# Performance work log

Measured on AMD Instinct MI355X. Metric: run time of the kernel, lower is better.

Reference implementation:

```python
import jax, jax.numpy as jnp
import numpy as np

N_ENT = 100000   # n_entities
N_HE = 20000     # n_hyperedges
D = 128          # embed_dim (in_dim == out_dim)
NNZ_A = 1600000  # nnz of A_in (~16 per row)
NNZ_H = 1000000  # nnz of each hyperedge incidence matrix


def spmm(rows, cols, vals, x, n_rows):
    """COO sparse (n_rows, n_cols) @ dense x (n_cols, D) -> (n_rows, D)."""
    msgs = vals[:, None] * x[cols]  # [nnz, D] gather + scale
    return jax.ops.segment_sum(msgs, rows, num_segments=n_rows)


def setup_inputs() -> dict:
    key = jax.random.key(0)
    ks = jax.random.split(key, 18)
    ego = jax.random.normal(ks[0], (N_ENT, D), dtype=jnp.float32)
    a_rows = jax.random.randint(ks[1], (NNZ_A,), 0, N_ENT)
    a_cols = jax.random.randint(ks[2], (NNZ_A,), 0, N_ENT)
    a_vals = jax.random.uniform(ks[3], (NNZ_A,), dtype=jnp.float32)
    p1_rows = jax.random.randint(ks[4], (NNZ_H,), 0, N_HE)
    p1_cols = jax.random.randint(ks[5], (NNZ_H,), 0, N_ENT)
    p1_vals = jax.random.uniform(ks[6], (NNZ_H,), dtype=jnp.float32)
    p2_rows = jax.random.randint(ks[7], (NNZ_H,), 0, N_ENT)
    p2_cols = jax.random.randint(ks[8], (NNZ_H,), 0, N_HE)
    p2_vals = jax.random.uniform(ks[9], (NNZ_H,), dtype=jnp.float32)
    l1_rows = jax.random.randint(ks[10], (NNZ_H,), 0, N_HE)
    l1_cols = jax.random.randint(ks[11], (NNZ_H,), 0, N_ENT)
    l1_vals = jax.random.uniform(ks[12], (NNZ_H,), dtype=jnp.float32)
    l2_rows = jax.random.randint(ks[13], (NNZ_H,), 0, N_ENT)
    l2_cols = jax.random.randint(ks[14], (NNZ_H,), 0, N_HE)
    l2_vals = jax.random.uniform(ks[15], (NNZ_H,), dtype=jnp.float32)
    W1 = jax.random.normal(ks[16], (D, D), dtype=jnp.float32) * 0.05
    b1 = jnp.zeros((D,), dtype=jnp.float32)
    W2 = jax.random.normal(ks[17], (D, D), dtype=jnp.float32) * 0.05
    b2 = jnp.zeros((D,), dtype=jnp.float32)
    return dict(ego=ego, a_rows=a_rows, a_cols=a_cols, a_vals=a_vals,
                p1_rows=p1_rows, p1_cols=p1_cols, p1_vals=p1_vals,
                p2_rows=p2_rows, p2_cols=p2_cols, p2_vals=p2_vals,
                l1_rows=l1_rows, l1_cols=l1_cols, l1_vals=l1_vals,
                l2_rows=l2_rows, l2_cols=l2_cols, l2_vals=l2_vals,
                W1=W1, b1=b1, W2=W2, b2=b2)


def reference(ego, a_rows, a_cols, a_vals,
              p1_rows, p1_cols, p1_vals,
              p2_rows, p2_cols, p2_vals,
              l1_rows, l1_cols, l1_vals,
              l2_rows, l2_cols, l2_vals,
              W1, b1, W2, b2):
    # side = A_in @ ego
    side = spmm(a_rows, a_cols, a_vals, ego, N_ENT)
    # proj = norm_proj2 @ (norm_proj1 @ ego)
    proj = spmm(p2_rows, p2_cols, p2_vals,
                spmm(p1_rows, p1_cols, p1_vals, ego, N_HE), N_ENT)
    # lib = norm_lib2 @ (norm_lib1 @ ego)
    lib = spmm(l2_rows, l2_cols, l2_vals,
               spmm(l1_rows, l1_cols, l1_vals, ego, N_HE), N_ENT)
    side = side + proj + lib
    # bi-interaction aggregator (PyTorch Linear: x @ W.T + b), LeakyReLU slope 0.01
    sum_emb = jax.nn.leaky_relu((ego + side) @ W1.T + b1)
    bi_emb = jax.nn.leaky_relu((ego * side) @ W2.T + b2)
    # attention=True -> sum of both branches; dropout is identity in eval
    return sum_emb + bi_emb
```

## Files before the change

### kernel.cpp

```cpp
#include <hip/hip_runtime.h>

#define N_ENT 100000
#define N_HE  20000
#define DD    128

#define RB_A   0
#define RB_P1  100000
#define RB_P2  120000
#define RB_L1  220000
#define RB_L2  240000
#define NROWS_TOT 340000

#define NB 452
#define TILE 3072
#define EPT  12

typedef float f32x4 __attribute__((ext_vector_type(4)));
typedef short bf16x8 __attribute__((ext_vector_type(8)));

__device__ __forceinline__ int bucket_region(int b) {
    return (b < 98) ? 0 : (b < 177) ? 1 : (b < 275) ? 2 : (b < 354) ? 3 : 4;
}
__device__ __forceinline__ int seg_shift(int s)      { return (s == 1 || s == 3) ? 8 : 10; }
__device__ __forceinline__ int seg_bucketbase(int s) { return s == 0 ? 0 : s == 1 ? 98 : s == 2 ? 177 : s == 3 ? 275 : 354; }
__device__ __forceinline__ int seg_cap(int s)        { return s == 0 ? 17408 : (s == 1 || s == 3) ? 13824 : 11264; }
__device__ __forceinline__ long long seg_arenabase(int s) {
    return s == 0 ? 0LL : s == 1 ? 1705984LL : s == 2 ? 2798080LL : s == 3 ? 3901952LL : 4994048LL;
}
__device__ __forceinline__ int seg_rowbase(int s)    { return s == 0 ? 0 : s == 1 ? 100000 : s == 2 ? 120000 : s == 3 ? 220000 : 240000; }
__device__ __forceinline__ int seg_rows(int s)       { return (s == 1 || s == 3) ? 20000 : 100000; }

__device__ __forceinline__ float bf_lo(unsigned u) { return __uint_as_float(u << 16); }
__device__ __forceinline__ float bf_hi(unsigned u) { return __uint_as_float(u & 0xffff0000u); }
__device__ __forceinline__ unsigned short f2bf(float f) {
    unsigned u = __float_as_uint(f);
    unsigned r = (u + 0x7fffu + ((u >> 16) & 1u)) >> 16;
    return (unsigned short)r;
}
__device__ __forceinline__ unsigned pack_bf16(float a, float b) {
    return (unsigned)f2bf(a) | ((unsigned)f2bf(b) << 16);
}
__device__ __forceinline__ float lrelu(float x) { return x > 0.0f ? x : 0.01f * x; }
__device__ __forceinline__ float i8f(unsigned u, int b) {
    return (float)((int)(u << (24 - 8 * b)) >> 24);
}

__global__ __launch_bounds__(256) void quant_ego_kernel(
    const float* __restrict__ ego, unsigned* __restrict__ ego_q,
    float* __restrict__ ego_scale)
{
    int row = (blockIdx.x * 256 + threadIdx.x) >> 5;
    if (row >= N_ENT) return;
    int l = threadIdx.x & 31;
    const float4 v = *(const float4*)(ego + (long long)row * DD + l * 4);
    float m = fmaxf(fmaxf(fabsf(v.x), fabsf(v.y)), fmaxf(fabsf(v.z), fabsf(v.w)));
    for (int d = 1; d < 32; d <<= 1) m = fmaxf(m, __shfl_xor(m, d, 32));
    float inv = (m > 0.0f) ? 127.0f / m : 0.0f;
    int q0 = __float2int_rn(v.x * inv);
    int q1 = __float2int_rn(v.y * inv);
    int q2 = __float2int_rn(v.z * inv);
    int q3 = __float2int_rn(v.w * inv);
    unsigned pk = (q0 & 255) | ((q1 & 255) << 8) | ((q2 & 255) << 16) | ((q3 & 255) << 24);
    ego_q[row * 32 + l] = pk;
    if (l == 0) ego_scale[row] = m * (1.0f / 127.0f);
}

struct BuildArgs {
    const int*   rows[5];
    const int*   cols[5];
    const float* vals[5];
    int nnzbase[6];
};

__device__ __forceinline__ void seg_of(int i, const int* nnzbase, int& seg, int& li) {
    int s = 0;
    s += (i >= nnzbase[1]);
    s += (i >= nnzbase[2]);
    s += (i >= nnzbase[3]);
    s += (i >= nnzbase[4]);
    seg = s; li = i - nnzbase[s];
}

__global__ __launch_bounds__(256, 4) void partition_kernel(
    BuildArgs a, int* __restrict__ gcursor, int2* __restrict__ arena)
{
    __shared__ int2 staging[TILE];
    __shared__ unsigned short posb[TILE];
    __shared__ int  hist[NB];
    __shared__ int  excl[NB + 1];
    __shared__ int  cursor[NB];
    __shared__ int  gofs[NB];

    const int t = threadIdx.x;
    const int tile_base = blockIdx.x * TILE;
    const int total = a.nnzbase[5];
    int tile_n = total - tile_base;
    if (tile_n > TILE) tile_n = TILE;
    if (tile_n <= 0) return;

    for (int i = t; i < NB; i += 256) hist[i] = 0;
    __syncthreads();

    int pk[EPT];
#pragma unroll
    for (int q = 0; q < EPT; ++q) {
        int j = t + q * 256;
        pk[q] = -1;
        if (j < tile_n) {
            int i = tile_base + j;
            int seg, li; seg_of(i, a.nnzbase, seg, li);
            int row = a.rows[seg][li];
            int sh = seg_shift(seg);
            int b = seg_bucketbase(seg) + (row >> sh);
            int rl = row & ((1 << sh) - 1);
            pk[q] = (b << 10) | rl;
            atomicAdd(&hist[b], 1);
        }
    }
    __syncthreads();

    if (t < 64) {
        int carry = 0;
        for (int base = 0; base < NB; base += 64) {
            int idx = base + t;
            int v = (idx < NB) ? hist[idx] : 0;
            int inc = v;
            for (int d = 1; d < 64; d <<= 1) {
                int u = __shfl_up(inc, d, 64);
                if (t >= d) inc += u;
            }
            if (idx < NB) excl[idx] = carry + inc - v;
            carry += __shfl(inc, 63, 64);
        }
        if (t == 0) excl[NB] = carry;
    }
    __syncthreads();

    for (int b = t; b < NB; b += 256) {
        int c = hist[b];
        int e = excl[b];
        int gb = (c > 0) ? atomicAdd(&gcursor[b], c) : 0;
        cursor[b] = e;
        gofs[b] = gb - e;
    }
    __syncthreads();

#pragma unroll
    for (int q = 0; q < EPT; ++q) {
        int j = t + q * 256;
        if (j < tile_n) {
            int i = tile_base + j;
            int seg, li; seg_of(i, a.nnzbase, seg, li);
            int col = a.cols[seg][li];
            float v = a.vals[seg][li];
            int b = pk[q] >> 10;
            int rl = pk[q] & 1023;
            int pos = atomicAdd(&cursor[b], 1);
            staging[pos] = make_int2((rl << 17) | col, __float_as_int(v));
        }
    }
    __syncthreads();

    for (int b = t; b < NB; b += 256) {
        int lo = excl[b], hi = excl[b + 1];
        for (int p = lo; p < hi; ++p) posb[p] = (unsigned short)b;
    }
    __syncthreads();

    for (int p = t; p < tile_n; p += 256) {
        int b = posb[p];
        int reg = bucket_region(b);
        long long slot = seg_arenabase(reg) + (long long)(b - seg_bucketbase(reg)) * seg_cap(reg);
        arena[slot + gofs[b] + p] = staging[p];
    }
}

__global__ __launch_bounds__(512) void bucket_scan_kernel(
    const int* __restrict__ gcursor, int* __restrict__ bbase, int* __restrict__ rp)
{
    __shared__ int tmp[512];
    int t = threadIdx.x;
    int v = (t < NB) ? gcursor[t] : 0;
    tmp[t] = v;
    __syncthreads();
    for (int d = 1; d < 512; d <<= 1) {
        int u = (t >= d) ? tmp[t - d] : 0;
        __syncthreads();
        tmp[t] += u;
        __syncthreads();
    }
    if (t < NB) bbase[t] = tmp[t] - v;
    if (t == NB - 1) rp[NROWS_TOT] = tmp[t];
}

__global__ __launch_bounds__(256) void bucket_sort_kernel(
    const int* __restrict__ gcursor, const int* __restrict__ bbase,
    const int2* __restrict__ arena, const float* __restrict__ ego_scale,
    int2* __restrict__ cv, int* __restrict__ rp)
{
    __shared__ int hist[1024];
    __shared__ int excl[1024];
    __shared__ int wsum[4];

    const int b = blockIdx.x;
    const int t = threadIdx.x;
    const int reg = bucket_region(b);
    const int sh = seg_shift(reg);
    const int stride = 1 << sh;
    const int lb = b - seg_bucketbase(reg);
    const int row_base_local = lb << sh;
    int nrows = seg_rows(reg) - row_base_local;
    if (nrows > stride) nrows = stride;
    const long long slot = seg_arenabase(reg) + (long long)lb * seg_cap(reg);
    const int count = gcursor[b];
    const int fbase = bbase[b];
    const bool fold = (reg == 0) || (reg == 1) || (reg == 3);

    for (int i = t; i < 1024; i += 256) hist[i] = 0;
    __syncthreads();

    for (int j = t; j < count; j += 256) {
        int key = arena[slot + j].x;
        atomicAdd(&hist[key >> 17], 1);
    }
    __syncthreads();

    {
        const int lane = t & 63, wave = t >> 6;
        int v[4]; int s = 0;
#pragma unroll
        for (int q = 0; q < 4; ++q) { v[q] = hist[t * 4 + q]; s += v[q]; }
        int inc = s;
        for (int d = 1; d < 64; d <<= 1) {
            int u = __shfl_up(inc, d, 64);
            if (lane >= d) inc += u;
        }
        if (lane == 63) wsum[wave] = inc;
        __syncthreads();
        int woff = 0;
        for (int w = 0; w < wave; ++w) woff += wsum[w];
        int run = woff + inc - s;
#pragma unroll
        for (int q = 0; q < 4; ++q) { excl[t * 4 + q] = run; run += v[q]; }
    }
    __syncthreads();

    const int grow0 = seg_rowbase(reg) + row_base_local;
    for (int r = t; r < nrows; r += 256)
        rp[grow0 + r] = fbase + excl[r];
    __syncthreads();

    for (int j = t; j < count; j += 256) {
        int2 e = arena[slot + j];
        int r = e.x >> 17;
        int c = e.x & 0x1FFFF;
        float v = __int_as_float(e.y);
        if (fold) v *= ego_scale[c];
        int pos = atomicAdd(&excl[r], 1);
        cv[fbase + pos] = make_int2(c, __float_as_int(v));
    }
}

__device__ __forceinline__ void walk_row_i8(
    const int2* __restrict__ cv, int start, int end, int lane,
    const unsigned* __restrict__ xq, float* acc)
{
    const int g  = lane >> 4;
    const int p8 = (lane & 15) * 2;

    for (int sb = start; sb < end; sb += 64) {
        int nn = end - sb; if (nn > 64) nn = 64;
        int2 mycv = make_int2(0, 0);
        if (lane < nn) mycv = cv[sb + lane];
        const int nn1 = nn - 1;
#pragma unroll 2
        for (int jb = 0; jb < nn; jb += 4) {
            int idx  = jb + g;
            int idxc = idx < nn1 ? idx : nn1;
            int   cs = __shfl(mycv.x, idxc, 64);
            float vs = __shfl(__int_as_float(mycv.y), idxc, 64);
            vs = (idx <= nn1) ? vs : 0.0f;
            const uint2 u = *reinterpret_cast<const uint2*>(xq + cs * 32 + p8);
            acc[0] = fmaf(vs, i8f(u.x, 0), acc[0]);
            acc[1] = fmaf(vs, i8f(u.x, 1), acc[1]);
            acc[2] = fmaf(vs, i8f(u.x, 2), acc[2]);
            acc[3] = fmaf(vs, i8f(u.x, 3), acc[3]);
            acc[4] = fmaf(vs, i8f(u.y, 0), acc[4]);
            acc[5] = fmaf(vs, i8f(u.y, 1), acc[5]);
            acc[6] = fmaf(vs, i8f(u.y, 2), acc[6]);
            acc[7] = fmaf(vs, i8f(u.y, 3), acc[7]);
        }
    }
}

__device__ __forceinline__ void walk_row_bf(
    const int2* __restrict__ cv, int start, int end, int lane,
    const unsigned* __restrict__ xb, float* acc)
{
    const int g   = lane >> 4;
    const int p16 = (lane & 15) * 4;

    for (int sb = start; sb < end; sb += 64) {
        int nn = end - sb; if (nn > 64) nn = 64;
        int2 mycv = make_int2(0, 0);
        if (lane < nn) mycv = cv[sb + lane];
        const int nn1 = nn - 1;
#pragma unroll 2
        for (int jb = 0; jb < nn; jb += 4) {
            int idx  = jb + g;
            int idxc = idx < nn1 ? idx : nn1;
            int   cs = __shfl(mycv.x, idxc, 64);
            float vs = __shfl(__int_as_float(mycv.y), idxc, 64);
            vs = (idx <= nn1) ? vs : 0.0f;
            const uint4 u = *reinterpret_cast<const uint4*>(xb + cs * 64 + p16);
            acc[0] = fmaf(vs, bf_lo(u.x), acc[0]);
            acc[1] = fmaf(vs, bf_hi(u.x), acc[1]);
            acc[2] = fmaf(vs, bf_lo(u.y), acc[2]);
            acc[3] = fmaf(vs, bf_hi(u.y), acc[3]);
            acc[4] = fmaf(vs, bf_lo(u.z), acc[4]);
            acc[5] = fmaf(vs, bf_hi(u.z), acc[5]);
            acc[6] = fmaf(vs, bf_lo(u.w), acc[6]);
            acc[7] = fmaf(vs, bf_hi(u.w), acc[7]);
        }
    }
}

__device__ __forceinline__ void reduce_groups(float* acc)
{
#pragma unroll
    for (int e = 0; e < 8; ++e) {
        acc[e] += __shfl_xor(acc[e], 16, 64);
        acc[e] += __shfl_xor(acc[e], 32, 64);
    }
}

__global__ __launch_bounds__(256) void spmm_stage1_kernel(
    const int* __restrict__ rp, const int2* __restrict__ cv,
    const unsigned* __restrict__ ego_q,
    unsigned* __restrict__ h1, unsigned* __restrict__ h2)
{
    int wid = (blockIdx.x * 256 + threadIdx.x) >> 6;
    int lane = threadIdx.x & 63;
    if (wid >= 2 * N_HE) return;
    int rbase; unsigned* y;
    if (wid < N_HE) { rbase = RB_P1 + wid;           y = h1 + wid * 64; }
    else            { rbase = RB_L1 + (wid - N_HE);  y = h2 + (wid - N_HE) * 64; }

    float acc[8] = {0, 0, 0, 0, 0, 0, 0, 0};
    walk_row_i8(cv, rp[rbase], rp[rbase + 1], lane, ego_q, acc);
    reduce_groups(acc);

    if (lane < 16) {
        uint4 o;
        o.x = pack_bf16(acc[0], acc[1]);
        o.y = pack_bf16(acc[2], acc[3]);
        o.z = pack_bf16(acc[4], acc[5]);
        o.w = pack_bf16(acc[6], acc[7]);
        *reinterpret_cast<uint4*>(y + lane * 4) = o;
    }
}

__global__ __launch_bounds__(256) void spmm_stage2_kernel(
    const int* __restrict__ rp, const int2* __restrict__ cv,
    const unsigned* __restrict__ ego_q,
    const unsigned* __restrict__ h1, const unsigned* __restrict__ h2,
    float* __restrict__ side)
{
    int wid = (blockIdx.x * 256 + threadIdx.x) >> 6;
    int lane = threadIdx.x & 63;
    if (wid >= N_ENT) return;

    float acc[8] = {0, 0, 0, 0, 0, 0, 0, 0};
    walk_row_i8(cv, rp[RB_A  + wid], rp[RB_A  + wid + 1], lane, ego_q, acc);
    walk_row_bf(cv, rp[RB_P2 + wid], rp[RB_P2 + wid + 1], lane, h1, acc);
    walk_row_bf(cv, rp[RB_L2 + wid], rp[RB_L2 + wid + 1], lane, h2, acc);
    reduce_groups(acc);

    if (lane < 16) {
        float* yp = side + (long long)wid * DD + (lane & 15) * 8;
        float4 a0 = make_float4(acc[0], acc[1], acc[2], acc[3]);
        float4 a1 = make_float4(acc[4], acc[5], acc[6], acc[7]);
        *reinterpret_cast<float4*>(yp)     = a0;
        *reinterpret_cast<float4*>(yp + 4) = a1;
    }
}

union BfFrag { unsigned u[4]; bf16x8 v; };

__global__ __launch_bounds__(512, 4) void dense_mfma_kernel(
    const float* __restrict__ ego, const float* __restrict__ side,
    const float* __restrict__ W1, const float* __restrict__ b1,
    const float* __restrict__ W2, const float* __restrict__ b2,
    float* __restrict__ out)
{
    __shared__ unsigned Wb1[8192];
    __shared__ unsigned Wb2[8192];

    const int tid = threadIdx.x;

    for (int idx = tid; idx < 8192; idx += 512) {
        int row = idx >> 6, pc = idx & 63;
        unsigned pk1 = pack_bf16(W1[row * 128 + pc * 2], W1[row * 128 + pc * 2 + 1]);
        unsigned pk2 = pack_bf16(W2[row * 128 + pc * 2], W2[row * 128 + pc * 2 + 1]);
        int boff = row * 256 + ((pc * 4) ^ ((row & 7) << 4));
        *(unsigned*)((char*)Wb1 + boff) = pk1;
        *(unsigned*)((char*)Wb2 + boff) = pk2;
    }
    __syncthreads();

    const int wave = tid >> 6;
    const int lane = tid & 63;
    const int m    = lane & 15;
    const int kg   = lane >> 4;

    float bs[8], bb[8];
#pragma unroll
    for (int c = 0; c < 8; ++c) {
        bs[c] = b1[c * 16 + m];
        bb[c] = b2[c * 16 + m];
    }

    for (int wt = blockIdx.x * 8 + wave; wt < 6250; wt += gridDim.x * 8) {
        const long long r0 = (long long)(wt * 16 + m) * DD;

        f32x4 accS[8], accB[8];
#pragma unroll
        for (int c = 0; c < 8; ++c) { accS[c] = (f32x4)0.0f; accB[c] = (f32x4)0.0f; }

#pragma unroll 1
        for (int kk = 0; kk < 4; ++kk) {
            const int kb = kk * 32 + kg * 8;

            float4 ea = *(const float4*)(ego  + r0 + kb);
            float4 eb = *(const float4*)(ego  + r0 + kb + 4);
            float4 sa = *(const float4*)(side + r0 + kb);
            float4 sb = *(const float4*)(side + r0 + kb + 4);

            BfFrag aS, aB;
            aS.u[0] = pack_bf16(ea.x + sa.x, ea.y + sa.y);
            aS.u[1] = pack_bf16(ea.z + sa.z, ea.w + sa.w);
            aS.u[2] = pack_bf16(eb.x + sb.x, eb.y + sb.y);
            aS.u[3] = pack_bf16(eb.z + sb.z, eb.w + sb.w);
            aB.u[0] = pack_bf16(ea.x * sa.x, ea.y * sa.y);
            aB.u[1] = pack_bf16(ea.z * sa.z, ea.w * sa.w);
            aB.u[2] = pack_bf16(eb.x * sb.x, eb.y * sb.y);
            aB.u[3] = pack_bf16(eb.z * sb.z, eb.w * sb.w);

#pragma unroll
            for (int c = 0; c < 8; ++c) {
                int wrow = c * 16 + m;
                int boff = wrow * 256 + ((kk * 64 + (kg << 4)) ^ ((wrow & 7) << 4));
                bf16x8 w1 = *(const bf16x8*)((const char*)Wb1 + boff);
                bf16x8 w2 = *(const bf16x8*)((const char*)Wb2 + boff);
                accS[c] = __builtin_amdgcn_mfma_f32_16x16x32_bf16(aS.v, w1, accS[c], 0, 0, 0);
                accB[c] = __builtin_amdgcn_mfma_f32_16x16x32_bf16(aB.v, w2, accB[c], 0, 0, 0);
            }
        }

#pragma unroll
        for (int c = 0; c < 8; ++c) {
#pragma unroll
            for (int q = 0; q < 4; ++q) {
                int orow = wt * 16 + kg * 4 + q;
                out[(long long)orow * DD + c * 16 + m] =
                    lrelu(accS[c][q] + bs[c]) + lrelu(accB[c][q] + bb[c]);
            }
        }
    }
}

extern "C" void kernel_launch(void* const* d_in, const int* in_sizes, int n_in,
                              void* d_out, int out_size, void* d_ws, size_t ws_size,
                              hipStream_t stream)
{
    const float* ego = (const float*)d_in[0];
    const float* W1  = (const float*)d_in[16];
    const float* b1  = (const float*)d_in[17];
    const float* W2  = (const float*)d_in[18];
    const float* b2  = (const float*)d_in[19];

    BuildArgs a;
    a.rows[0] = (const int*)d_in[1];  a.cols[0] = (const int*)d_in[2];  a.vals[0] = (const float*)d_in[3];
    a.rows[1] = (const int*)d_in[4];  a.cols[1] = (const int*)d_in[5];  a.vals[1] = (const float*)d_in[6];
    a.rows[2] = (const int*)d_in[7];  a.cols[2] = (const int*)d_in[8];  a.vals[2] = (const float*)d_in[9];
    a.rows[3] = (const int*)d_in[10]; a.cols[3] = (const int*)d_in[11]; a.vals[3] = (const float*)d_in[12];
    a.rows[4] = (const int*)d_in[13]; a.cols[4] = (const int*)d_in[14]; a.vals[4] = (const float*)d_in[15];
    int nnz[5] = { in_sizes[1], in_sizes[4], in_sizes[7], in_sizes[10], in_sizes[13] };
    a.nnzbase[0] = 0;
    for (int s = 0; s < 5; ++s) a.nnzbase[s + 1] = a.nnzbase[s] + nnz[s];
    const int total = a.nnzbase[5];

    char* p = (char*)d_ws;
    float*    side     = (float*)p;
    int2*     arena    = (int2*)p;        p += (size_t)N_ENT * DD * 4;
    unsigned* ego_q    = (unsigned*)p;    p += (size_t)N_ENT * 32 * 4;
    float*    ego_scale= (float*)p;       p += (size_t)100096 * 4;
    unsigned* h1       = (unsigned*)p;    p += (size_t)N_HE * 64 * 4;
    unsigned* h2       = (unsigned*)p;    p += (size_t)N_HE * 64 * 4;
    int2*     cv       = (int2*)p;        p += (size_t)total * 8;
    int*      rp       = (int*)p;         p += 340224 * 4;
    int*      gcursor  = (int*)p;         p += 512 * 4;
    int*      bbase    = (int*)p;         p += 512 * 4;

    hipMemsetAsync(gcursor, 0, NB * sizeof(int), stream);
    quant_ego_kernel<<<(N_ENT * 32 + 255) / 256, 256, 0, stream>>>(ego, ego_q, ego_scale);
    const int nblk_part = (total + TILE - 1) / TILE;
    partition_kernel<<<nblk_part, 256, 0, stream>>>(a, gcursor, arena);
    bucket_scan_kernel<<<1, 512, 0, stream>>>(gcursor, bbase, rp);
    bucket_sort_kernel<<<NB, 256, 0, stream>>>(gcursor, bbase, arena, ego_scale, cv, rp);

    spmm_stage1_kernel<<<(2 * N_HE) / 4, 256, 0, stream>>>(rp, cv, ego_q, h1, h2);
    spmm_stage2_kernel<<<N_ENT / 4, 256, 0, stream>>>(rp, cv, ego_q, h1, h2, side);

    dense_mfma_kernel<<<782, 512, 0, stream>>>(ego, side, W1, b1, W2, b2, (float*)d_out);
}
```

Baseline: 376.8 us.

## Merge second-stage SpMMs into one combined CSR over int8-quantized stacked features

Builds a single combined CSR for the final-stage rows, with the A, P2 and L2 entries merged per entity row. Their columns index into one stacked feature table: ego plus the two hyperedge intermediates. The stage-1 outputs are quantized to int8 with a per-row scale instead of bf16, so stage 2 walks each row once with a single int8 gather path. The walk is also reshaped so 8 groups of 8 lanes each load 16 bytes, and the per-column scale is applied at walk time instead of being folded during sort. This cuts stage-2 row walks from three to one and shrinks intermediate traffic, at the cost of extra int8 quantization error on the hyperedge intermediates and a per-edge scale load.

```diff
diff --git a/kernel.cpp b/kernel.cpp
--- a/kernel.cpp
+++ b/kernel.cpp
@@ -4,14 +4,16 @@
 #define N_HE  20000
 #define DD    128
 
-#define RB_A   0
-#define RB_P1  100000
-#define RB_P2  120000
-#define RB_L1  220000
-#define RB_L2  240000
-#define NROWS_TOT 340000
-
-#define NB 452
+#define XROW_H1 100000
+#define XROW_H2 120000
+#define NXROWS  140000
+
+#define RP_S2  0
+#define RP_P1  100001
+#define RP_L1  120002
+#define RP_LEN 140803
+
+#define NB 354
 #define TILE 3072
 #define EPT  12
 
@@ -19,19 +21,17 @@
 typedef short bf16x8 __attribute__((ext_vector_type(8)));
 
 __device__ __forceinline__ int bucket_region(int b) {
-    return (b < 98) ? 0 : (b < 177) ? 1 : (b < 275) ? 2 : (b < 354) ? 3 : 4;
-}
-__device__ __forceinline__ int seg_shift(int s)      { return (s == 1 || s == 3) ? 8 : 10; }
-__device__ __forceinline__ int seg_bucketbase(int s) { return s == 0 ? 0 : s == 1 ? 98 : s == 2 ? 177 : s == 3 ? 275 : 354; }
-__device__ __forceinline__ int seg_cap(int s)        { return s == 0 ? 17408 : (s == 1 || s == 3) ? 13824 : 11264; }
-__device__ __forceinline__ long long seg_arenabase(int s) {
-    return s == 0 ? 0LL : s == 1 ? 1705984LL : s == 2 ? 2798080LL : s == 3 ? 3901952LL : 4994048LL;
-}
-__device__ __forceinline__ int seg_rowbase(int s)    { return s == 0 ? 0 : s == 1 ? 100000 : s == 2 ? 120000 : s == 3 ? 220000 : 240000; }
-__device__ __forceinline__ int seg_rows(int s)       { return (s == 1 || s == 3) ? 20000 : 100000; }
-
-__device__ __forceinline__ float bf_lo(unsigned u) { return __uint_as_float(u << 16); }
-__device__ __forceinline__ float bf_hi(unsigned u) { return __uint_as_float(u & 0xffff0000u); }
+    return (b < 196) ? 0 : (b < 275) ? 1 : 2;
+}
+__device__ __forceinline__ int reg_shift(int r)      { return r == 0 ? 9 : 8; }
+__device__ __forceinline__ int reg_bucketbase(int r) { return r == 0 ? 0 : r == 1 ? 196 : 275; }
+__device__ __forceinline__ int reg_cap(int r)        { return r == 0 ? 19968 : 13824; }
+__device__ __forceinline__ long long reg_arenabase(int r) {
+    return r == 0 ? 0LL : r == 1 ? 3913728LL : 5005824LL;
+}
+__device__ __forceinline__ int reg_rpbase(int r)     { return r == 0 ? RP_S2 : r == 1 ? RP_P1 : RP_L1; }
+__device__ __forceinline__ int reg_rows(int r)       { return r == 0 ? 100000 : 20000; }
+
 __device__ __forceinline__ unsigned short f2bf(float f) {
     unsigned u = __float_as_uint(f);
     unsigned r = (u + 0x7fffu + ((u >> 16) & 1u)) >> 16;
@@ -46,8 +46,8 @@
 }
 
 __global__ __launch_bounds__(256) void quant_ego_kernel(
-    const float* __restrict__ ego, unsigned* __restrict__ ego_q,
-    float* __restrict__ ego_scale)
+    const float* __restrict__ ego, unsigned* __restrict__ xq,
+    float* __restrict__ xs)
 {
     int row = (blockIdx.x * 256 + threadIdx.x) >> 5;
     if (row >= N_ENT) return;
@@ -61,8 +61,8 @@
     int q2 = __float2int_rn(v.z * inv);
     int q3 = __float2int_rn(v.w * inv);
     unsigned pk = (q0 & 255) | ((q1 & 255) << 8) | ((q2 & 255) << 16) | ((q3 & 255) << 24);
-    ego_q[row * 32 + l] = pk;
-    if (l == 0) ego_scale[row] = m * (1.0f / 127.0f);
+    xq[row * 32 + l] = pk;
+    if (l == 0) xs[row] = m * (1.0f / 127.0f);
 }
 
 struct BuildArgs {
@@ -71,6 +71,10 @@
     const float* vals[5];
     int nnzbase[6];
 };
+
+__device__ __forceinline__ int seg_bbase(int s)  { return (s == 1) ? 196 : (s == 3) ? 275 : 0; }
+__device__ __forceinline__ int seg_shift2(int s) { return (s == 1 || s == 3) ? 8 : 9; }
+__device__ __forceinline__ int seg_colofs(int s) { return (s == 2) ? XROW_H1 : (s == 4) ? XROW_H2 : 0; }
 
 __device__ __forceinline__ void seg_of(int i, const int* nnzbase, int& seg, int& li) {
     int s = 0;
@@ -110,10 +114,10 @@
             int i = tile_base + j;
             int seg, li; seg_of(i, a.nnzbase, seg, li);
             int row = a.rows[seg][li];
-            int sh = seg_shift(seg);
-            int b = seg_bucketbase(seg) + (row >> sh);
+            int sh = seg_shift2(seg);
+            int b = seg_bbase(seg) + (row >> sh);
             int rl = row & ((1 << sh) - 1);
-            pk[q] = (b << 10) | rl;
+            pk[q] = (b << 9) | rl;
             atomicAdd(&hist[b], 1);
         }
     }
@@ -151,12 +155,12 @@
         if (j < tile_n) {
             int i = tile_base + j;
             int seg, li; seg_of(i, a.nnzbase, seg, li);
-            int col = a.cols[seg][li];
+            int colp = a.cols[seg][li] + seg_colofs(seg);
             float v = a.vals[seg][li];
-            int b = pk[q] >> 10;
-            int rl = pk[q] & 1023;
+            int b = pk[q] >> 9;
+            int rl = pk[q] & 511;
             int pos = atomicAdd(&cursor[b], 1);
-            staging[pos] = make_int2((rl << 17) | col, __float_as_int(v));
+            staging[pos] = make_int2((rl << 18) | colp, __float_as_int(v));
         }
     }
     __syncthreads();
@@ -170,7 +174,7 @@
     for (int p = t; p < tile_n; p += 256) {
         int b = posb[p];
         int reg = bucket_region(b);
-        long long slot = seg_arenabase(reg) + (long long)(b - seg_bucketbase(reg)) * seg_cap(reg);
+        long long slot = reg_arenabase(reg) + (long long)(b - reg_bucketbase(reg)) * reg_cap(reg);
         arena[slot + gofs[b] + p] = staging[p];
     }
 }
@@ -190,46 +194,45 @@
         __syncthreads();
     }
     if (t < NB) bbase[t] = tmp[t] - v;
-    if (t == NB - 1) rp[NROWS_TOT] = tmp[t];
+    if (t == 196) rp[RP_S2 + 100000] = tmp[t] - v;
+    if (t == 275) rp[RP_P1 + 20000]  = tmp[t] - v;
+    if (t == NB - 1) rp[RP_L1 + 20000] = tmp[t];
 }
 
 __global__ __launch_bounds__(256) void bucket_sort_kernel(
     const int* __restrict__ gcursor, const int* __restrict__ bbase,
-    const int2* __restrict__ arena, const float* __restrict__ ego_scale,
-    int2* __restrict__ cv, int* __restrict__ rp)
-{
-    __shared__ int hist[1024];
-    __shared__ int excl[1024];
+    const int2* __restrict__ arena, int2* __restrict__ cv, int* __restrict__ rp)
+{
+    __shared__ int hist[512];
+    __shared__ int excl[512];
     __shared__ int wsum[4];
 
     const int b = blockIdx.x;
     const int t = threadIdx.x;
     const int reg = bucket_region(b);
-    const int sh = seg_shift(reg);
+    const int sh = reg_shift(reg);
     const int stride = 1 << sh;
-    const int lb = b - seg_bucketbase(reg);
+    const int lb = b - reg_bucketbase(reg);
     const int row_base_local = lb << sh;
-    int nrows = seg_rows(reg) - row_base_local;
+    int nrows = reg_rows(reg) - row_base_local;
     if (nrows > stride) nrows = stride;
-    const long long slot = seg_arenabase(reg) + (long long)lb * seg_cap(reg);
+    const long long slot = reg_arenabase(reg) + (long long)lb * reg_cap(reg);
     const int count = gcursor[b];
     const int fbase = bbase[b];
-    const bool fold = (reg == 0) || (reg == 1) || (reg == 3);
-
-    for (int i = t; i < 1024; i += 256) hist[i] = 0;
+
+    for (int i = t; i < 512; i += 256) hist[i] = 0;
     __syncthreads();
 
     for (int j = t; j < count; j += 256) {
         int key = arena[slot + j].x;
-        atomicAdd(&hist[key >> 17], 1);
+        atomicAdd(&hist[key >> 18], 1);
     }
     __syncthreads();
 
     {
         const int lane = t & 63, wave = t >> 6;
-        int v[4]; int s = 0;
-#pragma unroll
-        for (int q = 0; q < 4; ++q) { v[q] = hist[t * 4 + q]; s += v[q]; }
+        int v0 = hist[t * 2], v1 = hist[t * 2 + 1];
+        int s = v0 + v1;
         int inc = s;
         for (int d = 1; d < 64; d <<= 1) {
             int u = __shfl_up(inc, d, 64);
@@ -240,95 +243,66 @@
         int woff = 0;
         for (int w = 0; w < wave; ++w) woff += wsum[w];
         int run = woff + inc - s;
-#pragma unroll
-        for (int q = 0; q < 4; ++q) { excl[t * 4 + q] = run; run += v[q]; }
-    }
-    __syncthreads();
-
-    const int grow0 = seg_rowbase(reg) + row_base_local;
+        excl[t * 2] = run;
+        excl[t * 2 + 1] = run + v0;
+    }
+    __syncthreads();
+
+    const int grow0 = reg_rpbase(reg) + row_base_local;
     for (int r = t; r < nrows; r += 256)
         rp[grow0 + r] = fbase + excl[r];
     __syncthreads();
 
     for (int j = t; j < count; j += 256) {
         int2 e = arena[slot + j];
-        int r = e.x >> 17;
-        int c = e.x & 0x1FFFF;
-        float v = __int_as_float(e.y);
-        if (fold) v *= ego_scale[c];
+        int r = e.x >> 18;
+        int c = e.x & 0x3FFFF;
         int pos = atomicAdd(&excl[r], 1);
-        cv[fbase + pos] = make_int2(c, __float_as_int(v));
-    }
-}
-
-__device__ __forceinline__ void walk_row_i8(
+        cv[fbase + pos] = make_int2(c, e.y);
+    }
+}
+
+__device__ __forceinline__ void walk_row8(
     const int2* __restrict__ cv, int start, int end, int lane,
-    const unsigned* __restrict__ xq, float* acc)
-{
-    const int g  = lane >> 4;
-    const int p8 = (lane & 15) * 2;
+    const unsigned* __restrict__ xq, const float* __restrict__ xs, float* acc)
+{
+    const int g = lane >> 3;
+    const int s = lane & 7;
 
     for (int sb = start; sb < end; sb += 64) {
         int nn = end - sb; if (nn > 64) nn = 64;
         int2 mycv = make_int2(0, 0);
-        if (lane < nn) mycv = cv[sb + lane];
+        float myv = 0.0f;
+        if (lane < nn) {
+            mycv = cv[sb + lane];
+            myv = __int_as_float(mycv.y) * xs[mycv.x];
+        }
         const int nn1 = nn - 1;
 #pragma unroll 2
-        for (int jb = 0; jb < nn; jb += 4) {
+        for (int jb = 0; jb < nn; jb += 8) {
             int idx  = jb + g;
             int idxc = idx < nn1 ? idx : nn1;
             int   cs = __shfl(mycv.x, idxc, 64);
-            float vs = __shfl(__int_as_float(mycv.y), idxc, 64);
+            float vs = __shfl(myv, idxc, 64);
             vs = (idx <= nn1) ? vs : 0.0f;
-            const uint2 u = *reinterpret_cast<const uint2*>(xq + cs * 32 + p8);
-            acc[0] = fmaf(vs, i8f(u.x, 0), acc[0]);
-            acc[1] = fmaf(vs, i8f(u.x, 1), acc[1]);
-            acc[2] = fmaf(vs, i8f(u.x, 2), acc[2]);
-            acc[3] = fmaf(vs, i8f(u.x, 3), acc[3]);
-            acc[4] = fmaf(vs, i8f(u.y, 0), acc[4]);
-            acc[5] = fmaf(vs, i8f(u.y, 1), acc[5]);
-            acc[6] = fmaf(vs, i8f(u.y, 2), acc[6]);
-            acc[7] = fmaf(vs, i8f(u.y, 3), acc[7]);
-        }
-    }
-}
-
-__device__ __forceinline__ void walk_row_bf(
-    const int2* __restrict__ cv, int start, int end, int lane,
-    const unsigned* __restrict__ xb, float* acc)
-{
-    const int g   = lane >> 4;
-    const int p16 = (lane & 15) * 4;
-
-    for (int sb = start; sb < end; sb += 64) {
-        int nn = end - sb; if (nn > 64) nn = 64;
-        int2 mycv = make_int2(0, 0);
-        if (lane < nn) mycv = cv[sb + lane];
-        const int nn1 = nn - 1;
-#pragma unroll 2
-        for (int jb = 0; jb < nn; jb += 4) {
-            int idx  = jb + g;
-            int idxc = idx < nn1 ? idx : nn1;
-            int   cs = __shfl(mycv.x, idxc, 64);
-            float vs = __shfl(__int_as_float(mycv.y), idxc, 64);
-            vs = (idx <= nn1) ? vs : 0.0f;
-            const uint4 u = *reinterpret_cast<const uint4*>(xb + cs * 64 + p16);
-            acc[0] = fmaf(vs, bf_lo(u.x), acc[0]);
-            acc[1] = fmaf(vs, bf_hi(u.x), acc[1]);
-            acc[2] = fmaf(vs, bf_lo(u.y), acc[2]);
-            acc[3] = fmaf(vs, bf_hi(u.y), acc[3]);
-            acc[4] = fmaf(vs, bf_lo(u.z), acc[4]);
-            acc[5] = fmaf(vs, bf_hi(u.z), acc[5]);
-            acc[6] = fmaf(vs, bf_lo(u.w), acc[6]);
-            acc[7] = fmaf(vs, bf_hi(u.w), acc[7]);
-        }
-    }
-}
-
-__device__ __forceinline__ void reduce_groups(float* acc)
-{
-#pragma unroll
-    for (int e = 0; e < 8; ++e) {
+            const uint4 u = *reinterpret_cast<const uint4*>(xq + cs * 32 + s * 4);
+#pragma unroll
+            for (int w = 0; w < 4; ++w) {
+                unsigned uw = (&u.x)[w];
+                acc[w * 4 + 0] = fmaf(vs, i8f(uw, 0), acc[w * 4 + 0]);
+                acc[w * 4 + 1] = fmaf(vs, i8f(uw, 1), acc[w * 4 + 1]);
+                acc[w * 4 + 2] = fmaf(vs, i8f(uw, 2), acc[w * 4 + 2]);
+                acc[w * 4 + 3] = fmaf(vs, i8f(uw, 3), acc[w * 4 + 3]);
+            }
+        }
+    }
+}
+
+__device__ __forceinline__ void reduce_groups8(float* acc)
+{
+#pragma unroll
+    for (int e = 0; e < 16; ++e) {
+        acc[e] += __shfl_xor(acc[e], 8, 64);
         acc[e] += __shfl_xor(acc[e], 16, 64);
         acc[e] += __shfl_xor(acc[e], 32, 64);
     }
@@ -336,52 +310,65 @@
 
 __global__ __launch_bounds__(256) void spmm_stage1_kernel(
     const int* __restrict__ rp, const int2* __restrict__ cv,
-    const unsigned* __restrict__ ego_q,
-    unsigned* __restrict__ h1, unsigned* __restrict__ h2)
+    unsigned* __restrict__ xq, float* __restrict__ xs)
 {
     int wid = (blockIdx.x * 256 + threadIdx.x) >> 6;
     int lane = threadIdx.x & 63;
     if (wid >= 2 * N_HE) return;
-    int rbase; unsigned* y;
-    if (wid < N_HE) { rbase = RB_P1 + wid;           y = h1 + wid * 64; }
-    else            { rbase = RB_L1 + (wid - N_HE);  y = h2 + (wid - N_HE) * 64; }
-
-    float acc[8] = {0, 0, 0, 0, 0, 0, 0, 0};
-    walk_row_i8(cv, rp[rbase], rp[rbase + 1], lane, ego_q, acc);
-    reduce_groups(acc);
-
-    if (lane < 16) {
+    int rbase, xrow;
+    if (wid < N_HE) { rbase = RP_P1 + wid;           xrow = XROW_H1 + wid; }
+    else            { rbase = RP_L1 + (wid - N_HE);  xrow = XROW_H2 + (wid - N_HE); }
+
+    float acc[16];
+#pragma unroll
+    for (int e = 0; e < 16; ++e) acc[e] = 0.0f;
+    walk_row8(cv, rp[rbase], rp[rbase + 1], lane, xq, xs, acc);
+    reduce_groups8(acc);
+
+    float m = 0.0f;
+#pragma unroll
+    for (int e = 0; e < 16; ++e) m = fmaxf(m, fabsf(acc[e]));
+    m = fmaxf(m, __shfl_xor(m, 1, 64));
+    m = fmaxf(m, __shfl_xor(m, 2, 64));
+    m = fmaxf(m, __shfl_xor(m, 4, 64));
+    float inv = (m > 0.0f) ? 127.0f / m : 0.0f;
+
+    if (lane < 8) {
         uint4 o;
-        o.x = pack_bf16(acc[0], acc[1]);
-        o.y = pack_bf16(acc[2], acc[3]);
-        o.z = pack_bf16(acc[4], acc[5]);
-        o.w = pack_bf16(acc[6], acc[7]);
-        *reinterpret_cast<uint4*>(y + lane * 4) = o;
+#pragma unroll
+        for (int w = 0; w < 4; ++w) {
+            int q0 = __float2int_rn(acc[w * 4 + 0] * inv);
+            int q1 = __float2int_rn(acc[w * 4 + 1] * inv);
+            int q2 = __float2int_rn(acc[w * 4 + 2] * inv);
+            int q3 = __float2int_rn(acc[w * 4 + 3] * inv);
+            (&o.x)[w] = (q0 & 255) | ((q1 & 255) << 8) | ((q2 & 255) << 16) | ((q3 & 255) << 24);
+        }
+        *reinterpret_cast<uint4*>(xq + xrow * 32 + lane * 4) = o;
+        if (lane == 0) xs[xrow] = m * (1.0f / 127.0f);
     }
 }
 
 __global__ __launch_bounds__(256) void spmm_stage2_kernel(
     const int* __restrict__ rp, const int2* __restrict__ cv,
-    const unsigned* __restrict__ ego_q,
-    const unsigned* __restrict__ h1, const unsigned* __restrict__ h2,
+    const unsigned* __restrict__ xq, const float* __restrict__ xs,
     float* __restrict__ side)
 {
     int wid = (blockIdx.x * 256 + threadIdx.x) >> 6;
     int lane = threadIdx.x & 63;
     if (wid >= N_ENT) return;
 
-    float acc[8] = {0, 0, 0, 0, 0, 0, 0, 0};
-    walk_row_i8(cv, rp[RB_A  + wid], rp[RB_A  + wid + 1], lane, ego_q, acc);
-    walk_row_bf(cv, rp[RB_P2 + wid], rp[RB_P2 + wid + 1], lane, h1, acc);
-    walk_row_bf(cv, rp[RB_L2 + wid], rp[RB_L2 + wid + 1], lane, h2, acc);
-    reduce_groups(acc);
-
-    if (lane < 16) {
-        float* yp = side + (long long)wid * DD + (lane & 15) * 8;
-        float4 a0 = make_float4(acc[0], acc[1], acc[2], acc[3]);
-        float4 a1 = make_float4(acc[4], acc[5], acc[6], acc[7]);
-        *reinterpret_cast<float4*>(yp)     = a0;
-        *reinterpret_cast<float4*>(yp + 4) = a1;
+    float acc[16];
+#pragma unroll
+    for (int e = 0; e < 16; ++e) acc[e] = 0.0f;
+    walk_row8(cv, rp[wid], rp[wid + 1], lane, xq, xs, acc);
+    reduce_groups8(acc);
+
+    if (lane < 8) {
+        float* yp = side + (long long)wid * DD + lane * 16;
+#pragma unroll
+        for (int w = 0; w < 4; ++w)
+            *reinterpret_cast<float4*>(yp + w * 4) =
+                make_float4(acc[w * 4], acc[w * 4 + 1], acc[w * 4 + 2], acc[w * 4 + 3]);
     }
 }
 
@@ -491,26 +478,24 @@
     const int total = a.nnzbase[5];
 
     char* p = (char*)d_ws;
-    float*    side     = (float*)p;
-    int2*     arena    = (int2*)p;        p += (size_t)N_ENT * DD * 4;
-    unsigned* ego_q    = (unsigned*)p;    p += (size_t)N_ENT * 32 * 4;
-    float*    ego_scale= (float*)p;       p += (size_t)100096 * 4;
-    unsigned* h1       = (unsigned*)p;    p += (size_t)N_HE * 64 * 4;
-    unsigned* h2       = (unsigned*)p;    p += (size_t)N_HE * 64 * 4;
-    int2*     cv       = (int2*)p;        p += (size_t)total * 8;
-    int*      rp       = (int*)p;         p += 340224 * 4;
-    int*      gcursor  = (int*)p;         p += 512 * 4;
-    int*      bbase    = (int*)p;         p += 512 * 4;
+    float*    side    = (float*)p;
+    int2*     arena   = (int2*)p;         p += (size_t)N_ENT * DD * 4;
+    unsigned* xq      = (unsigned*)p;     p += (size_t)140032 * 32 * 4;
+    float*    xs      = (float*)p;        p += (size_t)140032 * 4;
+    int2*     cv      = (int2*)p;         p += (size_t)total * 8;
+    int*      rp      = (int*)p;          p += 141056 * 4;
+    int*      gcursor = (int*)p;          p += 512 * 4;
+    int*      bbase   = (int*)p;          p += 512 * 4;
 
     hipMemsetAsync(gcursor, 0, NB * sizeof(int), stream);
-    quant_ego_kernel<<<(N_ENT * 32 + 255) / 256, 256, 0, stream>>>(ego, ego_q, ego_scale);
+    quant_ego_kernel<<<(N_ENT * 32 + 255) / 256, 256, 0, stream>>>(ego, xq, xs);
     const int nblk_part = (total + TILE - 1) / TILE;
     partition_kernel<<<nblk_part, 256, 0, stream>>>(a, gcursor, arena);
     bucket_scan_kernel<<<1, 512, 0, stream>>>(gcursor, bbase, rp);
-    bucket_sort_kernel<<<NB, 256, 0, stream>>>(gcursor, bbase, arena, ego_scale, cv, rp);
-
-    spmm_stage1_kernel<<<(2 * N_HE) / 4, 256, 0, stream>>>(rp, cv, ego_q, h1, h2);
-    spmm_stage2_kernel<<<N_ENT / 4, 256, 0, stream>>>(rp, cv, ego_q, h1, h2, side);
+    bucket_sort_kernel<<<NB, 256, 0, stream>>>(gcursor, bbase, arena, cv, rp);
+
+    spmm_stage1_kernel<<<(2 * N_HE) / 4, 256, 0, stream>>>(rp, cv, xq, xs);
+    spmm_stage2_kernel<<<N_ENT / 4, 256, 0, stream>>>(rp, cv, xq, xs, side);
 
     dense_mfma_kernel<<<782, 512, 0, stream>>>(ego, side, W1, b1, W2, b2, (float*)d_out);
 }
```

Result: faster. 332.5 us (-11.8%).
